# Optimization experiments

Hardware: AMD Instinct MI355X
Metric: run time of the kernel (lower is better)

## Reference

```python
import jax, jax.numpy as jnp
import numpy as np

B, S, D, H = 2, 2048, 1024, 16
DH = D // H  # head dim = 64


def setup_inputs() -> dict:
    key = jax.random.key(0)
    ks = jax.random.split(key, 8)
    q = jax.random.normal(ks[0], (B, S, D), dtype=jnp.float32)
    k = jax.random.normal(ks[1], (B, S, D), dtype=jnp.float32)
    v = jax.random.normal(ks[2], (B, S, D), dtype=jnp.float32)
    attn_mask = jax.random.randint(ks[3], (1, 1, S, S), 0, 2, dtype=jnp.int32)
    sc = 1.0 / np.sqrt(D)
    Wq = (jax.random.normal(ks[4], (D, D), dtype=jnp.float32) * sc)
    Wk = (jax.random.normal(ks[5], (D, D), dtype=jnp.float32) * sc)
    Wv = (jax.random.normal(ks[6], (D, D), dtype=jnp.float32) * sc)
    Wo = (jax.random.normal(ks[7], (D, D), dtype=jnp.float32) * sc)
    return {"q": q, "k": k, "v": v, "attn_mask": attn_mask,
            "Wq": Wq, "Wk": Wk, "Wv": Wv, "Wo": Wo}


def reference(q, k, v, attn_mask, Wq, Wk, Wv, Wo):
    bs = q.shape[0]
    # torch Linear: y = x @ W.T ; split heads -> [B, H, S, DH]
    qh = (q @ Wq.T).reshape(bs, -1, H, DH).transpose(0, 2, 1, 3)
    kh = (k @ Wk.T).reshape(bs, -1, H, DH).transpose(0, 2, 1, 3)
    vh = (v @ Wv.T).reshape(bs, -1, H, DH).transpose(0, 2, 1, 3)
    # scaled dot-product attention with explicit [B,H,S,S] scores
    scores = jnp.einsum('bhqd,bhkd->bhqk', qh, kh) / jnp.sqrt(
        jnp.asarray(DH, dtype=qh.dtype))
    scores = jnp.where(attn_mask == 0, jnp.asarray(-1e34, scores.dtype), scores)
    attn = jax.nn.softmax(scores, axis=-1)
    out = jnp.einsum('bhqk,bhkd->bhqd', attn, vh)
    out = out.transpose(0, 2, 1, 3).reshape(bs, -1, H * DH)
    out = out @ Wo.T
    return (out, attn)
```

## Files before the change

### kernel.cpp

```cpp
#include <hip/hip_runtime.h>
#include <stdint.h>

#define S_ 2048
#define NKT_ 32
#define NKTA_ 16
#define LP 72

typedef short bf16x8 __attribute__((ext_vector_type(8)));
typedef float f32x4 __attribute__((ext_vector_type(4)));

__device__ __forceinline__ short f2bf(float x) {
  union { float f; uint32_t u; } v; v.f = x;
  uint32_t r = v.u + 0x7fffu + ((v.u >> 16) & 1u);
  return (short)(r >> 16);
}
__device__ __forceinline__ float bf2f(short s) {
  union { uint32_t u; float f; } v; v.u = ((uint32_t)(uint16_t)s) << 16;
  return v.f;
}

__device__ __forceinline__ void gload16(const void* g, void* l) {
  __builtin_amdgcn_global_load_lds((const __attribute__((address_space(1))) void*)g,
                                   (__attribute__((address_space(3))) void*)l, 16, 0, 0);
}

__global__ __launch_bounds__(256) void detect_dtype(const uint32_t* __restrict__ q,
                                                    uint32_t* __restrict__ flag) {
  __shared__ int cnt;
  int t = threadIdx.x;
  if (t == 0) cnt = 0;
  __syncthreads();
  uint32_t w = q[t];
  int e = (int)((w >> 7) & 0xFF);
  int hit = (e >= 100 && e <= 141) ? 1 : 0;
  atomicAdd(&cnt, hit);
  __syncthreads();
  if (t == 0) *flag = (cnt >= 200) ? 0u : 1u;
}

__device__ __forceinline__ void cvt_body(const void* __restrict__ src,
                                         short* __restrict__ d, long n8, int f) {
  long i = (long)blockIdx.x * 256 + threadIdx.x;
  const long stride = (long)gridDim.x * 256;
  if (f) {
    const f32x4* s = (const f32x4*)src;
    for (; i < n8; i += stride) {
      f32x4 a = s[2 * i], b = s[2 * i + 1];
      bf16x8 r;
      r[0] = f2bf(a[0]); r[1] = f2bf(a[1]); r[2] = f2bf(a[2]); r[3] = f2bf(a[3]);
      r[4] = f2bf(b[0]); r[5] = f2bf(b[1]); r[6] = f2bf(b[2]); r[7] = f2bf(b[3]);
      *(bf16x8*)(d + i * 8) = r;
    }
  } else {
    const bf16x8* s = (const bf16x8*)src;
    for (; i < n8; i += stride) *(bf16x8*)(d + i * 8) = s[i];
  }
}

__global__ __launch_bounds__(256) void to_bf16_batch(
    const void* __restrict__ q, const void* __restrict__ k, const void* __restrict__ v,
    const void* __restrict__ wq, const void* __restrict__ wk, const void* __restrict__ wv,
    short* __restrict__ dst, const uint32_t* __restrict__ flag) {
  const void* src; long n8; long doff;
  switch (blockIdx.y) {
    case 0:  src = q;  n8 = 524288; doff = 0;        break;
    case 1:  src = k;  n8 = 524288; doff = 4194304;  break;
    case 2:  src = v;  n8 = 524288; doff = 8388608;  break;
    case 3:  src = wq; n8 = 131072; doff = 12582912; break;
    case 4:  src = wk; n8 = 131072; doff = 13631488; break;
    default: src = wv; n8 = 131072; doff = 14680064; break;
  }
  cvt_body(src, dst + doff, n8, (int)*flag);
}

__global__ __launch_bounds__(256) void to_bf16_one(const void* __restrict__ src,
                                                   short* __restrict__ dst, long n8,
                                                   const uint32_t* __restrict__ flag) {
  cvt_body(src, dst, n8, (int)*flag);
}

template <int MODE>
__device__ __forceinline__ void gemm_body(short* sA, short* sW,
    const short* __restrict__ A, const short* __restrict__ W,
    short* __restrict__ dst, float* __restrict__ dstF, int outf) {
  const int tid = threadIdx.x;
  const int wave = tid >> 6, lane = tid & 63;
  const int quad = lane >> 4, l16 = lane & 15;
  const int m0 = blockIdx.x * 128, n0 = blockIdx.y * 128;
  const int wm = wave >> 1, wn = wave & 1;

  f32x4 acc[4][4] = {};

  for (int k0 = 0; k0 < 1024; k0 += 64) {
#pragma unroll
    for (int it = 0; it < 4; ++it) {
      int c = it * 256 + tid;
      int r = c >> 3, cs = (c & 7) ^ (r & 7);
      int ldsoff = (it * 256 + wave * 64) * 8;
      gload16(A + (long)(m0 + r) * 1024 + k0 + cs * 8, sA + ldsoff);
      gload16(W + (long)(n0 + r) * 1024 + k0 + cs * 8, sW + ldsoff);
    }
    __syncthreads();
    const short* Pa = (MODE == 2) ? sW : sA;
    const short* Pb = (MODE == 2) ? sA : sW;
#pragma unroll
    for (int kk = 0; kk < 2; ++kk) {
      const int cx = ((kk * 4 + quad) ^ (l16 & 7)) * 8;
      bf16x8 af[4], bfr[4];
#pragma unroll
      for (int i = 0; i < 4; ++i)
        af[i] = *(const bf16x8*)(Pa + (wm * 64 + i * 16 + l16) * 64 + cx);
#pragma unroll
      for (int j = 0; j < 4; ++j)
        bfr[j] = *(const bf16x8*)(Pb + (wn * 64 + j * 16 + l16) * 64 + cx);
#pragma unroll
      for (int i = 0; i < 4; ++i)
#pragma unroll
        for (int j = 0; j < 4; ++j)
          acc[i][j] = __builtin_amdgcn_mfma_f32_16x16x32_bf16(af[i], bfr[j], acc[i][j], 0, 0, 0);
    }
    __syncthreads();
  }

#pragma unroll
  for (int i = 0; i < 4; ++i)
#pragma unroll
    for (int j = 0; j < 4; ++j)
#pragma unroll
      for (int r = 0; r < 4; ++r) {
        float vv = acc[i][j][r];
        if (MODE == 0) vv *= 0.18033688011112042f;
        if (MODE == 2) {
          int n = n0 + wm * 64 + i * 16 + quad * 4 + r;
          int m = m0 + wn * 64 + j * 16 + l16;
          int b = m >> 11, s = m & 2047, h = n >> 6, dh = n & 63;
          dst[((long)((b * 16 + h) * 64 + dh)) * 2048 + s] = f2bf(vv);
        } else {
          int m = m0 + wm * 64 + i * 16 + quad * 4 + r;
          int n = n0 + wn * 64 + j * 16 + l16;
          if (MODE == 3) {
            if (outf) dstF[(long)m * 1024 + n] = vv;
            else      dst[(long)m * 1024 + n] = f2bf(vv);
          } else {
            int b = m >> 11, s = m & 2047, h = n >> 6, dh = n & 63;
            dst[((long)(b * 16 + h) * 2048 + s) * 64 + dh] = f2bf(vv);
          }
        }
      }
}

__global__ __launch_bounds__(256) void qkv_kernel(
    const short* __restrict__ qb, const short* __restrict__ kb, const short* __restrict__ vb,
    const short* __restrict__ Wqb, const short* __restrict__ Wkb, const short* __restrict__ Wvb,
    short* __restrict__ qh, short* __restrict__ kh, short* __restrict__ vt) {
  __shared__ __align__(16) short sA[128 * 64];
  __shared__ __align__(16) short sW[128 * 64];
  if (blockIdx.z == 0)      gemm_body<0>(sA, sW, qb, Wqb, qh, nullptr, 0);
  else if (blockIdx.z == 1) gemm_body<1>(sA, sW, kb, Wkb, kh, nullptr, 0);
  else                      gemm_body<2>(sA, sW, vb, Wvb, vt, nullptr, 0);
}

__global__ __launch_bounds__(256) void oproj_kernel(
    const short* __restrict__ o, const short* __restrict__ Wob,
    const uint32_t* __restrict__ flag,
    short* __restrict__ outB, float* __restrict__ outF) {
  __shared__ __align__(16) short sA[128 * 64];
  __shared__ __align__(16) short sW[128 * 64];
  gemm_body<3>(sA, sW, o, Wob, outB, outF, (int)*flag);
}

__global__ __launch_bounds__(256) void pack_mask(const int* __restrict__ mask,
                                                 uint32_t* __restrict__ bits) {
  int gt = blockIdx.x * 256 + threadIdx.x;
  int wid = gt >> 6, lane = gt & 63;
  int nw = (gridDim.x * 256) >> 6;
  for (int g = wid; g < (S_ * S_) / 64; g += nw) {
    int v = mask[(long)g * 64 + lane];
    unsigned long long b = __ballot(v != 0);
    if (lane == 0) bits[2 * g] = (uint32_t)b;
    if (lane == 1) bits[2 * g + 1] = (uint32_t)(b >> 32);
  }
}

__global__ __launch_bounds__(256) void attn_kernel(
    const short* __restrict__ qh, const short* __restrict__ kh,
    const short* __restrict__ vt, const uint32_t* __restrict__ mbits,
    const uint32_t* __restrict__ flag,
    short* __restrict__ attnB, float* __restrict__ attnF, short* __restrict__ o) {
  __shared__ __align__(16) short sK[2][64 * 64];
  __shared__ __align__(16) short sV[2][64 * 64];
  __shared__ __align__(16) short sP[4][32 * LP];
  const int tid = threadIdx.x;
  const int wave = tid >> 6, lane = tid & 63;
  const int quad = lane >> 4, l16 = lane & 15;
  const int bidf = blockIdx.y * 16 + blockIdx.x;
  const int bh = (bidf & 7) * 4 + ((bidf >> 3) >> 4);
  const int q0 = ((bidf >> 3) & 15) * 128;
  const int outf = (int)*flag;
  const short* Qb = qh + (long)bh * S_ * 64;
  const short* Kb = kh + (long)bh * S_ * 64;
  const short* Vb = vt + (long)bh * 64 * S_;
  short* attnBb = attnB + (long)bh * S_ * S_;
  float* attnFb = attnF + (long)bh * S_ * S_;
  short* sPw = sP[wave];
  const uint32_t cm0 = 1u << l16, cm1 = 1u << (l16 + 16);

  auto bufA = [&](int b) -> short* { return b ? &sV[0][0] : &sK[0][0]; };
  auto stageA = [&](int kt, int b) {
    short* dstp = bufA(b);
#pragma unroll
    for (int it = 0; it < 4; ++it) {
      int c = it * 256 + tid;
      int r = c >> 3, cs = (c & 7) ^ (r & 7);
      gload16(Kb + (long)(kt * 128 + r) * 64 + cs * 8, dstp + (it * 256 + wave * 64) * 8);
    }
  };
  auto stageK = [&](int kt, int b) {
#pragma unroll
    for (int it = 0; it < 2; ++it) {
      int c = it * 256 + tid;
      int r = c >> 3, cs = (c & 7) ^ (r & 7);
      gload16(Kb + (long)(kt * 64 + r) * 64 + cs * 8, &sK[b][(it * 256 + wave * 64) * 8]);
    }
  };
  auto stageV = [&](int kt, int b) {
#pragma unroll
    for (int it = 0; it < 2; ++it) {
      int c = it * 256 + tid;
      int r = c >> 3, cs = (c & 7) ^ (r & 7);
      gload16(Vb + (long)r * S_ + kt * 64 + cs * 8, &sV[b][(it * 256 + wave * 64) * 8]);
    }
  };

  bf16x8 qf[2][2];
#pragma unroll
  for (int i = 0; i < 2; ++i)
#pragma unroll
    for (int kk = 0; kk < 2; ++kk)
      qf[i][kk] = *(const bf16x8*)(Qb + (long)(q0 + wave * 32 + i * 16 + l16) * 64 + kk * 32 + quad * 8);

  float mrun[2][4], lrun[2][4];
#pragma unroll
  for (int i = 0; i < 2; ++i)
#pragma unroll
    for (int r = 0; r < 4; ++r) { mrun[i][r] = -3e38f; lrun[i][r] = 0.f; }

  stageA(0, 0);
  __syncthreads();
  int buf = 0;
  for (int kt = 0; kt < NKTA_; ++kt) {
    if (kt + 1 < NKTA_) stageA(kt + 1, buf ^ 1);
    const short* Kt = bufA(buf);
    f32x4 acc[2][8] = {};
#pragma unroll
    for (int kk = 0; kk < 2; ++kk) {
      const int cx = ((kk * 4 + quad) ^ (l16 & 7)) * 8;
      bf16x8 bfr[8];
#pragma unroll
      for (int j = 0; j < 8; ++j)
        bfr[j] = *(const bf16x8*)(Kt + (j * 16 + l16) * 64 + cx);
      __builtin_amdgcn_s_setprio(1);
#pragma unroll
      for (int i = 0; i < 2; ++i)
#pragma unroll
        for (int j = 0; j < 8; ++j)
          acc[i][j] = __builtin_amdgcn_mfma_f32_16x16x32_bf16(qf[i][kk], bfr[j], acc[i][j], 0, 0, 0);
      __builtin_amdgcn_s_setprio(0);
    }
#pragma unroll
    for (int i = 0; i < 2; ++i)
#pragma unroll
      for (int r = 0; r < 4; ++r) {
        int qrow = q0 + wave * 32 + i * 16 + quad * 4 + r;
        uint4 w = *(const uint4*)(mbits + qrow * 64 + kt * 4);
        float s0 = (w.x & cm0) ? acc[i][0][r] : -1e30f;
        float s1 = (w.x & cm1) ? acc[i][1][r] : -1e30f;
        float s2 = (w.y & cm0) ? acc[i][2][r] : -1e30f;
        float s3 = (w.y & cm1) ? acc[i][3][r] : -1e30f;
        float s4 = (w.z & cm0) ? acc[i][4][r] : -1e30f;
        float s5 = (w.z & cm1) ? acc[i][5][r] : -1e30f;
        float s6 = (w.w & cm0) ? acc[i][6][r] : -1e30f;
        float s7 = (w.w & cm1) ? acc[i][7][r] : -1e30f;
        float mx = fmaxf(fmaxf(fmaxf(s0, s1), fmaxf(s2, s3)),
                         fmaxf(fmaxf(s4, s5), fmaxf(s6, s7)));
        mx = fmaxf(mx, __shfl_xor(mx, 1));
        mx = fmaxf(mx, __shfl_xor(mx, 2));
        mx = fmaxf(mx, __shfl_xor(mx, 4));
        mx = fmaxf(mx, __shfl_xor(mx, 8));
        float mold = mrun[i][r];
        float mnew = fmaxf(mold, mx);
        float sum = exp2f(s0 - mnew) + exp2f(s1 - mnew) + exp2f(s2 - mnew) + exp2f(s3 - mnew)
                  + exp2f(s4 - mnew) + exp2f(s5 - mnew) + exp2f(s6 - mnew) + exp2f(s7 - mnew);
        sum += __shfl_xor(sum, 1);
        sum += __shfl_xor(sum, 2);
        sum += __shfl_xor(sum, 4);
        sum += __shfl_xor(sum, 8);
        lrun[i][r] = lrun[i][r] * exp2f(mold - mnew) + sum;
        mrun[i][r] = mnew;
      }
    __syncthreads();
    buf ^= 1;
  }

  float invl[2][4];
#pragma unroll
  for (int i = 0; i < 2; ++i)
#pragma unroll
    for (int r = 0; r < 4; ++r) invl[i][r] = 1.0f / lrun[i][r];

  f32x4 acco[2][4] = {};

  stageK(0, 0); stageV(0, 0);
  __syncthreads();
  buf = 0;
  for (int kt = 0; kt < NKT_; ++kt) {
    const int k0 = kt * 64;
    if (kt + 1 < NKT_) { stageK(kt + 1, buf ^ 1); stageV(kt + 1, buf ^ 1); }
    f32x4 acc[2][4] = {};
#pragma unroll
    for (int kk = 0; kk < 2; ++kk) {
      const int cx = ((kk * 4 + quad) ^ (l16 & 7)) * 8;
      bf16x8 bfr[4];
#pragma unroll
      for (int j = 0; j < 4; ++j)
        bfr[j] = *(const bf16x8*)(&sK[buf][(j * 16 + l16) * 64 + cx]);
      __builtin_amdgcn_s_setprio(1);
#pragma unroll
      for (int i = 0; i < 2; ++i)
#pragma unroll
        for (int j = 0; j < 4; ++j)
          acc[i][j] = __builtin_amdgcn_mfma_f32_16x16x32_bf16(qf[i][kk], bfr[j], acc[i][j], 0, 0, 0);
      __builtin_amdgcn_s_setprio(0);
    }
#pragma unroll
    for (int i = 0; i < 2; ++i)
#pragma unroll
      for (int r = 0; r < 4; ++r) {
        int qrow = q0 + wave * 32 + i * 16 + quad * 4 + r;
        const uint32_t* wp = mbits + qrow * 64 + (k0 >> 5);
        uint32_t w0 = wp[0], w1 = wp[1];
        float mm = mrun[i][r], il = invl[i][r];
        float s0 = (w0 & cm0) ? acc[i][0][r] : -1e30f;
        float s1 = (w0 & cm1) ? acc[i][1][r] : -1e30f;
        float s2 = (w1 & cm0) ? acc[i][2][r] : -1e30f;
        float s3 = (w1 & cm1) ? acc[i][3][r] : -1e30f;
        int rowL = i * 16 + quad * 4 + r;
        short* rp = sPw + rowL * LP;
        rp[0  + l16] = f2bf(exp2f(s0 - mm) * il);
        rp[16 + l16] = f2bf(exp2f(s1 - mm) * il);
        rp[32 + l16] = f2bf(exp2f(s2 - mm) * il);
        rp[48 + l16] = f2bf(exp2f(s3 - mm) * il);
      }
    asm volatile("s_waitcnt lgkmcnt(0)" ::: "memory");
    __builtin_amdgcn_sched_barrier(0);
#pragma unroll
    for (int it = 0; it < 4; ++it) {
      int cid = it * 64 + lane;
      int rowL = cid >> 3, kc = cid & 7;
      bf16x8 vals = *(const bf16x8*)(sPw + rowL * LP + kc * 8);
      long base = (long)(q0 + wave * 32 + rowL) * S_ + k0 + kc * 8;
      if (outf) {
        f32x4 lo, hi;
#pragma unroll
        for (int e = 0; e < 4; ++e) { lo[e] = bf2f(vals[e]); hi[e] = bf2f(vals[e + 4]); }
        *(f32x4*)(attnFb + base) = lo;
        *(f32x4*)(attnFb + base + 4) = hi;
      } else {
        *(bf16x8*)(attnBb + base) = vals;
      }
    }
    bf16x8 vf[2][4];
#pragma unroll
    for (int kk = 0; kk < 2; ++kk) {
      const int cx = ((kk * 4 + quad) ^ (l16 & 7)) * 8;
#pragma unroll
      for (int jd = 0; jd < 4; ++jd)
        vf[kk][jd] = *(const bf16x8*)(&sV[buf][(jd * 16 + l16) * 64 + cx]);
    }
    __builtin_amdgcn_s_setprio(1);
#pragma unroll
    for (int kk = 0; kk < 2; ++kk)
#pragma unroll
      for (int i = 0; i < 2; ++i) {
        bf16x8 pf = *(const bf16x8*)(sPw + (i * 16 + l16) * LP + (kk * 4 + quad) * 8);
#pragma unroll
        for (int jd = 0; jd < 4; ++jd)
          acco[i][jd] = __builtin_amdgcn_mfma_f32_16x16x32_bf16(pf, vf[kk][jd], acco[i][jd], 0, 0, 0);
      }
    __builtin_amdgcn_s_setprio(0);
    __syncthreads();
    buf ^= 1;
  }

  const int b = bh >> 4, h = bh & 15;
#pragma unroll
  for (int i = 0; i < 2; ++i)
#pragma unroll
    for (int jd = 0; jd < 4; ++jd)
#pragma unroll
      for (int r = 0; r < 4; ++r) {
        int qrow = q0 + wave * 32 + i * 16 + quad * 4 + r;
        int dh = jd * 16 + l16;
        o[(long)(b * S_ + qrow) * 1024 + h * 64 + dh] = f2bf(acco[i][jd][r]);
      }
}

extern "C" void kernel_launch(void* const* d_in, const int* in_sizes, int n_in,
                              void* d_out, int out_size, void* d_ws, size_t ws_size,
                              hipStream_t stream) {
  (void)in_sizes; (void)n_in; (void)out_size; (void)ws_size;
  const void* q  = d_in[0];
  const void* k  = d_in[1];
  const void* v  = d_in[2];
  const int* mask = (const int*)d_in[3];
  const void* Wq = d_in[4];
  const void* Wk = d_in[5];
  const void* Wv = d_in[6];
  const void* Wo = d_in[7];

  short* outB  = (short*)d_out;
  short* attnB = outB + (long)4194304;
  float* outF  = (float*)d_out;
  float* attnF = outF + (long)4194304;

  short* qh = (short*)d_ws;
  short* kh = qh + (long)4194304;
  short* vt = kh + (long)4194304;
  short* o  = vt + (long)4194304;
  uint32_t* mbits = (uint32_t*)(o + (long)4194304);
  uint32_t* flag  = mbits + 131072;

  short* qb  = (short*)((char*)d_out + (20l << 20));
  short* kb  = qb  + (long)4194304;
  short* vb  = kb  + (long)4194304;
  short* wqb = vb  + (long)4194304;
  short* wkb = wqb + (long)1048576;
  short* wvb = wkb + (long)1048576;
  short* wob = qh;

  detect_dtype<<<dim3(1), dim3(256), 0, stream>>>((const uint32_t*)q, flag);
  pack_mask<<<dim3(256), dim3(256), 0, stream>>>(mask, mbits);
  to_bf16_batch<<<dim3(512, 6), dim3(256), 0, stream>>>(q, k, v, Wq, Wk, Wv, qb, flag);
  qkv_kernel<<<dim3(32, 8, 3), dim3(256), 0, stream>>>(qb, kb, vb, wqb, wkb, wvb, qh, kh, vt);
  attn_kernel<<<dim3(16, 32), dim3(256), 0, stream>>>(qh, kh, vt, mbits, flag, attnB, attnF, o);
  to_bf16_one<<<dim3(512), dim3(256), 0, stream>>>(Wo, wob, 131072, flag);
  oproj_kernel<<<dim3(32, 8), dim3(256), 0, stream>>>(o, wob, flag, outB, outF);
}
```

Before: 859.5 us.

## Split attention into stats and output kernels with smaller query tiles

```diff
diff --git a/kernel.cpp b/kernel.cpp
--- a/kernel.cpp
+++ b/kernel.cpp
@@ -182,20 +182,118 @@
   }
 }
 
-__global__ __launch_bounds__(256) void attn_kernel(
+__global__ __launch_bounds__(256) void attn_a(
+    const short* __restrict__ qh, const short* __restrict__ kh,
+    const uint32_t* __restrict__ mbits, float* __restrict__ ml) {
+  __shared__ __align__(16) short sKa[2][128 * 64];
+  const int tid = threadIdx.x;
+  const int wave = tid >> 6, lane = tid & 63;
+  const int quad = lane >> 4, l16 = lane & 15;
+  const int bid = blockIdx.x;
+  const int within = bid >> 3;
+  const int bh = (bid & 7) * 4 + (within >> 5);
+  const int q0 = (within & 31) * 64;
+  const short* Qb = qh + (long)bh * S_ * 64;
+  const short* Kb = kh + (long)bh * S_ * 64;
+  const uint32_t cm0 = 1u << l16, cm1 = 1u << (l16 + 16);
+
+  auto stageA = [&](int kt, int b) {
+    short* dstp = &sKa[b][0];
+#pragma unroll
+    for (int it = 0; it < 4; ++it) {
+      int c = it * 256 + tid;
+      int r = c >> 3, cs = (c & 7) ^ (r & 7);
+      gload16(Kb + (long)(kt * 128 + r) * 64 + cs * 8, dstp + (it * 256 + wave * 64) * 8);
+    }
+  };
+
+  bf16x8 qf[2];
+#pragma unroll
+  for (int kk = 0; kk < 2; ++kk)
+    qf[kk] = *(const bf16x8*)(Qb + (long)(q0 + wave * 16 + l16) * 64 + kk * 32 + quad * 8);
+
+  float mrun[4], lrun[4];
+#pragma unroll
+  for (int r = 0; r < 4; ++r) { mrun[r] = -3e38f; lrun[r] = 0.f; }
+
+  stageA(0, 0);
+  __syncthreads();
+  int buf = 0;
+  for (int kt = 0; kt < NKTA_; ++kt) {
+    if (kt + 1 < NKTA_) stageA(kt + 1, buf ^ 1);
+    const short* Kt = &sKa[buf][0];
+    f32x4 acc[8] = {};
+#pragma unroll
+    for (int kk = 0; kk < 2; ++kk) {
+      const int cx = ((kk * 4 + quad) ^ (l16 & 7)) * 8;
+      bf16x8 bfr[8];
+#pragma unroll
+      for (int j = 0; j < 8; ++j)
+        bfr[j] = *(const bf16x8*)(Kt + (j * 16 + l16) * 64 + cx);
+      __builtin_amdgcn_s_setprio(1);
+#pragma unroll
+      for (int j = 0; j < 8; ++j)
+        acc[j] = __builtin_amdgcn_mfma_f32_16x16x32_bf16(qf[kk], bfr[j], acc[j], 0, 0, 0);
+      __builtin_amdgcn_s_setprio(0);
+    }
+#pragma unroll
+    for (int r = 0; r < 4; ++r) {
+      int qrow = q0 + wave * 16 + quad * 4 + r;
+      uint4 w = *(const uint4*)(mbits + qrow * 64 + kt * 4);
+      float s0 = (w.x & cm0) ? acc[0][r] : -1e30f;
+      float s1 = (w.x & cm1) ? acc[1][r] : -1e30f;
+      float s2 = (w.y & cm0) ? acc[2][r] : -1e30f;
+      float s3 = (w.y & cm1) ? acc[3][r] : -1e30f;
+      float s4 = (w.z & cm0) ? acc[4][r] : -1e30f;
+      float s5 = (w.z & cm1) ? acc[5][r] : -1e30f;
+      float s6 = (w.w & cm0) ? acc[6][r] : -1e30f;
+      float s7 = (w.w & cm1) ? acc[7][r] : -1e30f;
+      float mx = fmaxf(fmaxf(fmaxf(s0, s1), fmaxf(s2, s3)),
+                       fmaxf(fmaxf(s4, s5), fmaxf(s6, s7)));
+      mx = fmaxf(mx, __shfl_xor(mx, 1));
+      mx = fmaxf(mx, __shfl_xor(mx, 2));
+      mx = fmaxf(mx, __shfl_xor(mx, 4));
+      mx = fmaxf(mx, __shfl_xor(mx, 8));
+      float mold = mrun[r];
+      float mnew = fmaxf(mold, mx);
+      float sum = exp2f(s0 - mnew) + exp2f(s1 - mnew) + exp2f(s2 - mnew) + exp2f(s3 - mnew)
+                + exp2f(s4 - mnew) + exp2f(s5 - mnew) + exp2f(s6 - mnew) + exp2f(s7 - mnew);
+      sum += __shfl_xor(sum, 1);
+      sum += __shfl_xor(sum, 2);
+      sum += __shfl_xor(sum, 4);
+      sum += __shfl_xor(sum, 8);
+      lrun[r] = lrun[r] * exp2f(mold - mnew) + sum;
+      mrun[r] = mnew;
+    }
+    __syncthreads();
+    buf ^= 1;
+  }
+
+  if (l16 == 0) {
+#pragma unroll
+    for (int r = 0; r < 4; ++r) {
+      int qrow = q0 + wave * 16 + quad * 4 + r;
+      ml[((long)bh * S_ + qrow) * 2]     = mrun[r];
+      ml[((long)bh * S_ + qrow) * 2 + 1] = 1.0f / lrun[r];
+    }
+  }
+}
+
+__global__ __launch_bounds__(256) void attn_b(
     const short* __restrict__ qh, const short* __restrict__ kh,
     const short* __restrict__ vt, const uint32_t* __restrict__ mbits,
-    const uint32_t* __restrict__ flag,
+    const float* __restrict__ ml, const uint32_t* __restrict__ flag,
     short* __restrict__ attnB, float* __restrict__ attnF, short* __restrict__ o) {
   __shared__ __align__(16) short sK[2][64 * 64];
   __shared__ __align__(16) short sV[2][64 * 64];
-  __shared__ __align__(16) short sP[4][32 * LP];
+  __shared__ __align__(16) short sP[4][16 * LP];
   const int tid = threadIdx.x;
   const int wave = tid >> 6, lane = tid & 63;
   const int quad = lane >> 4, l16 = lane & 15;
-  const int bidf = blockIdx.y * 16 + blockIdx.x;
-  const int bh = (bidf & 7) * 4 + ((bidf >> 3) >> 4);
-  const int q0 = ((bidf >> 3) & 15) * 128;
+  const int bid = blockIdx.x;
+  const int within = bid >> 3;
+  const int bh = (bid & 7) * 4 + (within >> 5);
+  const int q0 = (within & 31) * 64;
   const int outf = (int)*flag;
   const short* Qb = qh + (long)bh * S_ * 64;
   const short* Kb = kh + (long)bh * S_ * 64;
@@ -205,16 +303,6 @@
   short* sPw = sP[wave];
   const uint32_t cm0 = 1u << l16, cm1 = 1u << (l16 + 16);
 
-  auto bufA = [&](int b) -> short* { return b ? &sV[0][0] : &sK[0][0]; };
-  auto stageA = [&](int kt, int b) {
-    short* dstp = bufA(b);
-#pragma unroll
-    for (int it = 0; it < 4; ++it) {
-      int c = it * 256 + tid;
-      int r = c >> 3, cs = (c & 7) ^ (r & 7);
-      gload16(Kb + (long)(kt * 128 + r) * 64 + cs * 8, dstp + (it * 256 + wave * 64) * 8);
-    }
-  };
   auto stageK = [&](int kt, int b) {
 #pragma unroll
     for (int it = 0; it < 2; ++it) {
@@ -232,91 +320,28 @@
     }
   };
 
-  bf16x8 qf[2][2];
-#pragma unroll
-  for (int i = 0; i < 2; ++i)
-#pragma unroll
-    for (int kk = 0; kk < 2; ++kk)
-      qf[i][kk] = *(const bf16x8*)(Qb + (long)(q0 + wave * 32 + i * 16 + l16) * 64 + kk * 32 + quad * 8);
-
-  float mrun[2][4], lrun[2][4];
-#pragma unroll
-  for (int i = 0; i < 2; ++i)
-#pragma unroll
-    for (int r = 0; r < 4; ++r) { mrun[i][r] = -3e38f; lrun[i][r] = 0.f; }
-
-  stageA(0, 0);
+  bf16x8 qf[2];
+#pragma unroll
+  for (int kk = 0; kk < 2; ++kk)
+    qf[kk] = *(const bf16x8*)(Qb + (long)(q0 + wave * 16 + l16) * 64 + kk * 32 + quad * 8);
+
+  float mr[4], il[4];
+#pragma unroll
+  for (int r = 0; r < 4; ++r) {
+    int qrow = q0 + wave * 16 + quad * 4 + r;
+    mr[r] = ml[((long)bh * S_ + qrow) * 2];
+    il[r] = ml[((long)bh * S_ + qrow) * 2 + 1];
+  }
+
+  f32x4 acco[4] = {};
+
+  stageK(0, 0); stageV(0, 0);
   __syncthreads();
   int buf = 0;
-  for (int kt = 0; kt < NKTA_; ++kt) {
-    if (kt + 1 < NKTA_) stageA(kt + 1, buf ^ 1);
-    const short* Kt = bufA(buf);
-    f32x4 acc[2][8] = {};
-#pragma unroll
-    for (int kk = 0; kk < 2; ++kk) {
-      const int cx = ((kk * 4 + quad) ^ (l16 & 7)) * 8;
-      bf16x8 bfr[8];
-#pragma unroll
-      for (int j = 0; j < 8; ++j)
-        bfr[j] = *(const bf16x8*)(Kt + (j * 16 + l16) * 64 + cx);
-      __builtin_amdgcn_s_setprio(1);
-#pragma unroll
-      for (int i = 0; i < 2; ++i)
-#pragma unroll
-        for (int j = 0; j < 8; ++j)
-          acc[i][j] = __builtin_amdgcn_mfma_f32_16x16x32_bf16(qf[i][kk], bfr[j], acc[i][j], 0, 0, 0);
-      __builtin_amdgcn_s_setprio(0);
-    }
-#pragma unroll
-    for (int i = 0; i < 2; ++i)
-#pragma unroll
-      for (int r = 0; r < 4; ++r) {
-        int qrow = q0 + wave * 32 + i * 16 + quad * 4 + r;
-        uint4 w = *(const uint4*)(mbits + qrow * 64 + kt * 4);
-        float s0 = (w.x & cm0) ? acc[i][0][r] : -1e30f;
-        float s1 = (w.x & cm1) ? acc[i][1][r] : -1e30f;
-        float s2 = (w.y & cm0) ? acc[i][2][r] : -1e30f;
-        float s3 = (w.y & cm1) ? acc[i][3][r] : -1e30f;
-        float s4 = (w.z & cm0) ? acc[i][4][r] : -1e30f;
-        float s5 = (w.z & cm1) ? acc[i][5][r] : -1e30f;
-        float s6 = (w.w & cm0) ? acc[i][6][r] : -1e30f;
-        float s7 = (w.w & cm1) ? acc[i][7][r] : -1e30f;
-        float mx = fmaxf(fmaxf(fmaxf(s0, s1), fmaxf(s2, s3)),
-                         fmaxf(fmaxf(s4, s5), fmaxf(s6, s7)));
-        mx = fmaxf(mx, __shfl_xor(mx, 1));
-        mx = fmaxf(mx, __shfl_xor(mx, 2));
-        mx = fmaxf(mx, __shfl_xor(mx, 4));
-        mx = fmaxf(mx, __shfl_xor(mx, 8));
-        float mold = mrun[i][r];
-        float mnew = fmaxf(mold, mx);
-        float sum = exp2f(s0 - mnew) + exp2f(s1 - mnew) + exp2f(s2 - mnew) + exp2f(s3 - mnew)
-                  + exp2f(s4 - mnew) + exp2f(s5 - mnew) + exp2f(s6 - mnew) + exp2f(s7 - mnew);
-        sum += __shfl_xor(sum, 1);
-        sum += __shfl_xor(sum, 2);
-        sum += __shfl_xor(sum, 4);
-        sum += __shfl_xor(sum, 8);
-        lrun[i][r] = lrun[i][r] * exp2f(mold - mnew) + sum;
-        mrun[i][r] = mnew;
-      }
-    __syncthreads();
-    buf ^= 1;
-  }
-
-  float invl[2][4];
-#pragma unroll
-  for (int i = 0; i < 2; ++i)
-#pragma unroll
-    for (int r = 0; r < 4; ++r) invl[i][r] = 1.0f / lrun[i][r];
-
-  f32x4 acco[2][4] = {};
-
-  stageK(0, 0); stageV(0, 0);
-  __syncthreads();
-  buf = 0;
   for (int kt = 0; kt < NKT_; ++kt) {
     const int k0 = kt * 64;
     if (kt + 1 < NKT_) { stageK(kt + 1, buf ^ 1); stageV(kt + 1, buf ^ 1); }
-    f32x4 acc[2][4] = {};
+    f32x4 acc[4] = {};
 #pragma unroll
     for (int kk = 0; kk < 2; ++kk) {
       const int cx = ((kk * 4 + quad) ^ (l16 & 7)) * 8;
@@ -326,47 +351,42 @@
         bfr[j] = *(const bf16x8*)(&sK[buf][(j * 16 + l16) * 64 + cx]);
       __builtin_amdgcn_s_setprio(1);
 #pragma unroll
-      for (int i = 0; i < 2; ++i)
-#pragma unroll
-        for (int j = 0; j < 4; ++j)
-          acc[i][j] = __builtin_amdgcn_mfma_f32_16x16x32_bf16(qf[i][kk], bfr[j], acc[i][j], 0, 0, 0);
+      for (int j = 0; j < 4; ++j)
+        acc[j] = __builtin_amdgcn_mfma_f32_16x16x32_bf16(qf[kk], bfr[j], acc[j], 0, 0, 0);
       __builtin_amdgcn_s_setprio(0);
     }
 #pragma unroll
-    for (int i = 0; i < 2; ++i)
-#pragma unroll
-      for (int r = 0; r < 4; ++r) {
-        int qrow = q0 + wave * 32 + i * 16 + quad * 4 + r;
-        const uint32_t* wp = mbits + qrow * 64 + (k0 >> 5);
-        uint32_t w0 = wp[0], w1 = wp[1];
-        float mm = mrun[i][r], il = invl[i][r];
-        float s0 = (w0 & cm0) ? acc[i][0][r] : -1e30f;
-        float s1 = (w0 & cm1) ? acc[i][1][r] : -1e30f;
-        float s2 = (w1 & cm0) ? acc[i][2][r] : -1e30f;
-        float s3 = (w1 & cm1) ? acc[i][3][r] : -1e30f;
-        int rowL = i * 16 + quad * 4 + r;
-        short* rp = sPw + rowL * LP;
-        rp[0  + l16] = f2bf(exp2f(s0 - mm) * il);
-        rp[16 + l16] = f2bf(exp2f(s1 - mm) * il);
-        rp[32 + l16] = f2bf(exp2f(s2 - mm) * il);
-        rp[48 + l16] = f2bf(exp2f(s3 - mm) * il);
-      }
+    for (int r = 0; r < 4; ++r) {
+      int qrow = q0 + wave * 16 + quad * 4 + r;
+      uint2 w = *(const uint2*)(mbits + qrow * 64 + kt * 2);
+      float mm = mr[r], sc = il[r];
+      float s0 = (w.x & cm0) ? acc[0][r] : -1e30f;
+      float s1 = (w.x & cm1) ? acc[1][r] : -1e30f;
+      float s2 = (w.y & cm0) ? acc[2][r] : -1e30f;
+      float s3 = (w.y & cm1) ? acc[3][r] : -1e30f;
+      int rowL = quad * 4 + r;
+      short* rp = sPw + rowL * LP;
+      rp[0  + l16] = f2bf(exp2f(s0 - mm) * sc);
+      rp[16 + l16] = f2bf(exp2f(s1 - mm) * sc);
+      rp[32 + l16] = f2bf(exp2f(s2 - mm) * sc);
+      rp[48 + l16] = f2bf(exp2f(s3 - mm) * sc);
+    }
     asm volatile("s_waitcnt lgkmcnt(0)" ::: "memory");
     __builtin_amdgcn_sched_barrier(0);
 #pragma unroll
-    for (int it = 0; it < 4; ++it) {
+    for (int it = 0; it < 2; ++it) {
       int cid = it * 64 + lane;
       int rowL = cid >> 3, kc = cid & 7;
       bf16x8 vals = *(const bf16x8*)(sPw + rowL * LP + kc * 8);
-      long base = (long)(q0 + wave * 32 + rowL) * S_ + k0 + kc * 8;
+      long base = (long)(q0 + wave * 16 + rowL) * S_ + k0 + kc * 8;
       if (outf) {
         f32x4 lo, hi;
 #pragma unroll
         for (int e = 0; e < 4; ++e) { lo[e] = bf2f(vals[e]); hi[e] = bf2f(vals[e + 4]); }
-        *(f32x4*)(attnFb + base) = lo;
-        *(f32x4*)(attnFb + base + 4) = hi;
+        __builtin_nontemporal_store(lo, (f32x4*)(attnFb + base));
+        __builtin_nontemporal_store(hi, (f32x4*)(attnFb + base + 4));
       } else {
-        *(bf16x8*)(attnBb + base) = vals;
+        __builtin_nontemporal_store(vals, (bf16x8*)(attnBb + base));
       }
     }
     bf16x8 vf[2][4];
@@ -379,14 +399,12 @@
     }
     __builtin_amdgcn_s_setprio(1);
 #pragma unroll
-    for (int kk = 0; kk < 2; ++kk)
-#pragma unroll
-      for (int i = 0; i < 2; ++i) {
-        bf16x8 pf = *(const bf16x8*)(sPw + (i * 16 + l16) * LP + (kk * 4 + quad) * 8);
-#pragma unroll
-        for (int jd = 0; jd < 4; ++jd)
-          acco[i][jd] = __builtin_amdgcn_mfma_f32_16x16x32_bf16(pf, vf[kk][jd], acco[i][jd], 0, 0, 0);
-      }
+    for (int kk = 0; kk < 2; ++kk) {
+      bf16x8 pf = *(const bf16x8*)(sPw + l16 * LP + (kk * 4 + quad) * 8);
+#pragma unroll
+      for (int jd = 0; jd < 4; ++jd)
+        acco[jd] = __builtin_amdgcn_mfma_f32_16x16x32_bf16(pf, vf[kk][jd], acco[jd], 0, 0, 0);
+    }
     __builtin_amdgcn_s_setprio(0);
     __syncthreads();
     buf ^= 1;
@@ -394,15 +412,13 @@
 
   const int b = bh >> 4, h = bh & 15;
 #pragma unroll
-  for (int i = 0; i < 2; ++i)
-#pragma unroll
-    for (int jd = 0; jd < 4; ++jd)
-#pragma unroll
-      for (int r = 0; r < 4; ++r) {
-        int qrow = q0 + wave * 32 + i * 16 + quad * 4 + r;
-        int dh = jd * 16 + l16;
-        o[(long)(b * S_ + qrow) * 1024 + h * 64 + dh] = f2bf(acco[i][jd][r]);
-      }
+  for (int jd = 0; jd < 4; ++jd)
+#pragma unroll
+    for (int r = 0; r < 4; ++r) {
+      int qrow = q0 + wave * 16 + quad * 4 + r;
+      int dh = jd * 16 + l16;
+      o[(long)(b * S_ + qrow) * 1024 + h * 64 + dh] = f2bf(acco[jd][r]);
+    }
 }
 
 extern "C" void kernel_launch(void* const* d_in, const int* in_sizes, int n_in,
@@ -430,6 +446,8 @@
   uint32_t* mbits = (uint32_t*)(o + (long)4194304);
   uint32_t* flag  = mbits + 131072;
 
+  float* ml = (float*)((char*)d_out + (4l << 20));
+
   short* qb  = (short*)((char*)d_out + (20l << 20));
   short* kb  = qb  + (long)4194304;
   short* vb  = kb  + (long)4194304;
@@ -442,7 +460,8 @@
   pack_mask<<<dim3(256), dim3(256), 0, stream>>>(mask, mbits);
   to_bf16_batch<<<dim3(512, 6), dim3(256), 0, stream>>>(q, k, v, Wq, Wk, Wv, qb, flag);
   qkv_kernel<<<dim3(32, 8, 3), dim3(256), 0, stream>>>(qb, kb, vb, wqb, wkb, wvb, qh, kh, vt);
-  attn_kernel<<<dim3(16, 32), dim3(256), 0, stream>>>(qh, kh, vt, mbits, flag, attnB, attnF, o);
+  attn_a<<<dim3(1024), dim3(256), 0, stream>>>(qh, kh, mbits, ml);
+  attn_b<<<dim3(1024), dim3(256), 0, stream>>>(qh, kh, vt, mbits, ml, flag, attnB, attnF, o);
   to_bf16_one<<<dim3(512), dim3(256), 0, stream>>>(Wo, wob, 131072, flag);
   oproj_kernel<<<dim3(32, 8), dim3(256), 0, stream>>>(o, wob, flag, outB, outF);
 }
```

Result: slower. 899.2 us (+4.6%).

## Write attention probabilities directly from registers and permute V layout to match

Applied to the files above, without the earlier changes.

```diff
diff --git a/kernel.cpp b/kernel.cpp
--- a/kernel.cpp
+++ b/kernel.cpp
@@ -7,6 +7,7 @@
 #define LP 72
 
 typedef short bf16x8 __attribute__((ext_vector_type(8)));
+typedef short bf16x4 __attribute__((ext_vector_type(4)));
 typedef float f32x4 __attribute__((ext_vector_type(4)));
 
 __device__ __forceinline__ short f2bf(float x) {
@@ -134,7 +135,8 @@
           int n = n0 + wm * 64 + i * 16 + quad * 4 + r;
           int m = m0 + wn * 64 + j * 16 + l16;
           int b = m >> 11, s = m & 2047, h = n >> 6, dh = n & 63;
-          dst[((long)((b * 16 + h) * 64 + dh)) * 2048 + s] = f2bf(vv);
+          int sp = (s & ~63) | (((s & 15) << 2) | ((s & 63) >> 4));
+          dst[((long)((b * 16 + h) * 64 + dh)) * 2048 + sp] = f2bf(vv);
         } else {
           int m = m0 + wm * 64 + i * 16 + quad * 4 + r;
           int n = n0 + wn * 64 + j * 16 + l16;
@@ -344,31 +346,29 @@
         float s1 = (w0 & cm1) ? acc[i][1][r] : -1e30f;
         float s2 = (w1 & cm0) ? acc[i][2][r] : -1e30f;
         float s3 = (w1 & cm1) ? acc[i][3][r] : -1e30f;
+        float p0 = exp2f(s0 - mm) * il;
+        float p1 = exp2f(s1 - mm) * il;
+        float p2 = exp2f(s2 - mm) * il;
+        float p3 = exp2f(s3 - mm) * il;
+        long base = (long)qrow * S_ + k0 + l16;
+        if (outf) {
+          __builtin_nontemporal_store(p0, attnFb + base);
+          __builtin_nontemporal_store(p1, attnFb + base + 16);
+          __builtin_nontemporal_store(p2, attnFb + base + 32);
+          __builtin_nontemporal_store(p3, attnFb + base + 48);
+        } else {
+          __builtin_nontemporal_store(f2bf(p0), attnBb + base);
+          __builtin_nontemporal_store(f2bf(p1), attnBb + base + 16);
+          __builtin_nontemporal_store(f2bf(p2), attnBb + base + 32);
+          __builtin_nontemporal_store(f2bf(p3), attnBb + base + 48);
+        }
+        bf16x4 pv;
+        pv[0] = f2bf(p0); pv[1] = f2bf(p1); pv[2] = f2bf(p2); pv[3] = f2bf(p3);
         int rowL = i * 16 + quad * 4 + r;
-        short* rp = sPw + rowL * LP;
-        rp[0  + l16] = f2bf(exp2f(s0 - mm) * il);
-        rp[16 + l16] = f2bf(exp2f(s1 - mm) * il);
-        rp[32 + l16] = f2bf(exp2f(s2 - mm) * il);
-        rp[48 + l16] = f2bf(exp2f(s3 - mm) * il);
+        *(bf16x4*)(sPw + rowL * LP + l16 * 4) = pv;
       }
     asm volatile("s_waitcnt lgkmcnt(0)" ::: "memory");
     __builtin_amdgcn_sched_barrier(0);
-#pragma unroll
-    for (int it = 0; it < 4; ++it) {
-      int cid = it * 64 + lane;
-      int rowL = cid >> 3, kc = cid & 7;
-      bf16x8 vals = *(const bf16x8*)(sPw + rowL * LP + kc * 8);
-      long base = (long)(q0 + wave * 32 + rowL) * S_ + k0 + kc * 8;
-      if (outf) {
-        f32x4 lo, hi;
-#pragma unroll
-        for (int e = 0; e < 4; ++e) { lo[e] = bf2f(vals[e]); hi[e] = bf2f(vals[e + 4]); }
-        *(f32x4*)(attnFb + base) = lo;
-        *(f32x4*)(attnFb + base + 4) = hi;
-      } else {
-        *(bf16x8*)(attnBb + base) = vals;
-      }
-    }
     bf16x8 vf[2][4];
 #pragma unroll
     for (int kk = 0; kk < 2; ++kk) {
```

Result: slower. 928.5 us (+8.0%).
